# Optimization experiments

Measured on AMD Instinct MI355X. Metric: run time of the kernel, lower is better.

## Reference

```python
import jax, jax.numpy as jnp
import numpy as np

EMBED_DIM = 192
NUM_HEADS = 6
HEAD_DIM = EMBED_DIM // NUM_HEADS
WIN = (7, 7, 7)
N = WIN[0] * WIN[1] * WIN[2]  # 343
B = 512
NW = 64  # windows per volume (mask leading dim); B % NW == 0
SCALE = HEAD_DIM ** (-0.5)


def _relative_position_index():
    coords = np.stack(np.meshgrid(np.arange(WIN[0]), np.arange(WIN[1]), np.arange(WIN[2]), indexing='ij'))
    flat = coords.reshape(3, -1)
    rel = flat[:, :, None] - flat[:, None, :]            # (3, N, N)
    rel = np.transpose(rel, (1, 2, 0)).astype(np.int64)  # (N, N, 3)
    rel[:, :, 0] += WIN[0] - 1
    rel[:, :, 1] += WIN[1] - 1
    rel[:, :, 2] += WIN[2] - 1
    rel[:, :, 0] *= (2 * WIN[1] - 1) * (2 * WIN[2] - 1)
    rel[:, :, 1] *= 2 * WIN[2] - 1
    return rel.sum(-1)  # (N, N) ints in [0, (2Wh-1)(2Ww-1)(2Wd-1))


def setup_inputs() -> dict:
    key = jax.random.key(0)
    ks = jax.random.split(key, 7)
    table_size = (2 * WIN[0] - 1) * (2 * WIN[1] - 1) * (2 * WIN[2] - 1)  # 2197
    return {
        'x': jax.random.normal(ks[0], (B, N, EMBED_DIM), dtype=jnp.float32),
        'mask': jax.random.normal(ks[1], (NW, N, N), dtype=jnp.float32),
        'qkv_w': jax.random.normal(ks[2], (EMBED_DIM, 3 * EMBED_DIM), dtype=jnp.float32) * 0.02,
        'qkv_b': jnp.zeros((3 * EMBED_DIM,), dtype=jnp.float32),
        'proj_w': jax.random.normal(ks[3], (EMBED_DIM, EMBED_DIM), dtype=jnp.float32) * 0.02,
        'proj_b': jnp.zeros((EMBED_DIM,), dtype=jnp.float32),
        'bias_table': jax.random.normal(ks[4], (table_size, NUM_HEADS), dtype=jnp.float32) * 0.02,
        'rpi': jnp.asarray(_relative_position_index(), dtype=jnp.int32),  # (N, N)
    }


def reference(x, mask, qkv_w, qkv_b, proj_w, proj_b, bias_table, rpi):
    Bn, Nn, C = x.shape
    # QKV projection
    qkv = x @ qkv_w + qkv_b                                   # (B, N, 3C)
    qkv = qkv.reshape(Bn, Nn, 3, NUM_HEADS, HEAD_DIM)
    qkv = jnp.transpose(qkv, (2, 0, 3, 1, 4))                 # (3, B, H, N, hd)
    q, k, v = qkv[0], qkv[1], qkv[2]
    attn = jnp.einsum('bhnd,bhmd->bhnm', q * SCALE, k)        # (B, H, N, N)
    # gather relative position bias: (N*N, H) -> (1, H, N, N)
    rel_bias = bias_table[rpi.reshape(-1)].reshape(Nn, Nn, NUM_HEADS)
    attn = attn + jnp.transpose(rel_bias, (2, 0, 1))[None]
    # per-window mask addition
    nw = mask.shape[0]
    attn = attn.reshape(Bn // nw, nw, NUM_HEADS, Nn, Nn)
    attn = attn + mask[None, :, None, :, :]
    attn = attn.reshape(Bn, NUM_HEADS, Nn, Nn)
    attn = jax.nn.softmax(attn, axis=-1)
    out = jnp.einsum('bhnm,bhmd->bnhd', attn, v).reshape(Bn, Nn, C)
    return out @ proj_w + proj_b
```

## Files before the change

kernel.cpp:

```cpp
#include <hip/hip_runtime.h>
#include <stdint.h>

#define N_TOK 343
#define NPAD  352
#define EMB   192
#define HD    32
#define SCALE 0.17677669529663689f

typedef __attribute__((ext_vector_type(8))) short short8;
typedef __attribute__((ext_vector_type(4))) short short4v;
typedef __attribute__((ext_vector_type(4))) float floatx4;

__device__ __forceinline__ short f2bf(float f) {
  union { float f; unsigned u; } v; v.f = f;
  unsigned r = v.u + 0x7fffu + ((v.u >> 16) & 1u);
  return (short)(r >> 16);
}
__device__ __forceinline__ float bf2f(short s) {
  union { unsigned u; float f; } v;
  v.u = ((unsigned)(unsigned short)s) << 16;
  return v.f;
}
__device__ __forceinline__ unsigned pack2(float a, float b) {
  return (unsigned)(unsigned short)f2bf(a) | ((unsigned)(unsigned short)f2bf(b) << 16);
}

__global__ void prep_weights(const float* __restrict__ qkv_w,
                             const float* __restrict__ qkv_b,
                             const float* __restrict__ proj_w,
                             short* __restrict__ wpack,
                             float* __restrict__ bpack,
                             short* __restrict__ WpT)
{
  int i0 = blockIdx.x * blockDim.x + threadIdx.x;
  int stride = gridDim.x * blockDim.x;
  for (int idx = i0; idx < 110592; idx += stride) {
    int k = idx % 192;
    int t = idx / 192;
    int n = t % 32;
    int mat = (t / 32) % 3;
    int h = t / 96;
    float v = qkv_w[k * 576 + mat * 192 + h * 32 + n];
    if (mat == 0) v *= SCALE;
    wpack[idx] = f2bf(v);
  }
  for (int idx = i0; idx < 36864; idx += stride) {
    int k = idx % 192;
    int n = idx / 192;
    WpT[idx] = f2bf(proj_w[k * 192 + n]);
  }
  for (int idx = i0; idx < 576; idx += stride) {
    int d = idx % 32;
    int mat = (idx / 32) % 3;
    int h = idx / 96;
    float v = qkv_b[mat * 192 + h * 32 + d];
    if (mat == 0) v *= SCALE;
    bpack[idx] = v;
  }
}

__global__ void prep_bias(const float* __restrict__ bias_table,
                          const int* __restrict__ rpi,
                          short* __restrict__ biasH)
{
  int p = blockIdx.x * blockDim.x + threadIdx.x;
  int h = blockIdx.y;
  if (p < N_TOK * N_TOK) {
    int t = rpi[p];
    biasH[h * (N_TOK * N_TOK) + p] = f2bf(bias_table[t * 6 + h]);
  }
}

__global__ __launch_bounds__(256, 2) void fused_attn(
    const float* __restrict__ x,
    const float* __restrict__ mask,
    const short* __restrict__ wpack,
    const float* __restrict__ bpack,
    const short* __restrict__ biasH,
    short* __restrict__ AO)
{
  const int tid  = threadIdx.x;
  const int wave = tid >> 6;
  const int lane = tid & 63;
  const int l16  = lane & 15;
  const int quad = lane >> 4;

  int id   = blockIdx.x;
  int xcd  = id & 7;
  int j    = id >> 3;
  int w_id = xcd * 8 + (j / 48);
  int r    = j % 48;
  int h    = r % 6;
  int b    = (r / 6) * 64 + w_id;

  extern __shared__ short smem_s[];
  short* Kl = smem_s;
  short* Vt = smem_s + 14080;
  short* Wv = smem_s + 25600 + wave * 2048;
  short* Qs = Wv;
  short* Pb = Wv + 640;

  const float* bsrc = bpack + h * 96;
  const float bq0 = bsrc[l16],      bq1 = bsrc[16 + l16];
  const float bk0 = bsrc[32 + l16], bk1 = bsrc[48 + l16];
  const float bv0 = bsrc[64 + l16], bv1 = bsrc[80 + l16];

  const float* xb = x + (size_t)b * (N_TOK * EMB);
  const short* wh = wpack + h * 18432;
  unsigned qreg[6][4];

#pragma unroll 1
  for (int ch = 0; ch < 6; ++ch) {
    int r0 = ch * 64 + wave * 16;
    if (r0 >= NPAD) continue;
    int row = r0 + l16;
    bool rok = row < N_TOK;
    const float* xr = xb + (size_t)row * EMB;

    short8 af[6];
#pragma unroll
    for (int kk = 0; kk < 6; ++kk) {
      const float* xp = xr + kk * 32 + quad * 8;
      float4 a0 = rok ? *(const float4*)xp       : make_float4(0.f, 0.f, 0.f, 0.f);
      float4 a1 = rok ? *(const float4*)(xp + 4) : make_float4(0.f, 0.f, 0.f, 0.f);
      short8 t;
      t[0] = f2bf(a0.x); t[1] = f2bf(a0.y); t[2] = f2bf(a0.z); t[3] = f2bf(a0.w);
      t[4] = f2bf(a1.x); t[5] = f2bf(a1.y); t[6] = f2bf(a1.z); t[7] = f2bf(a1.w);
      af[kk] = t;
    }

    int mg = r0 + quad * 4;
#pragma unroll
    for (int mat = 0; mat < 3; ++mat) {
      const short* wb = wh + mat * 6144;
      floatx4 acc0 = {0.f, 0.f, 0.f, 0.f}, acc1 = {0.f, 0.f, 0.f, 0.f};
#pragma unroll
      for (int kk = 0; kk < 6; ++kk) {
        short8 b0 = *(const short8*)(wb + l16 * 192 + kk * 32 + quad * 8);
        short8 b1 = *(const short8*)(wb + (16 + l16) * 192 + kk * 32 + quad * 8);
        acc0 = __builtin_amdgcn_mfma_f32_16x16x32_bf16(af[kk], b0, acc0, 0, 0, 0);
        acc1 = __builtin_amdgcn_mfma_f32_16x16x32_bf16(af[kk], b1, acc1, 0, 0, 0);
      }
      if (mat == 0) {
#pragma unroll
        for (int reg = 0; reg < 4; ++reg)
          qreg[ch][reg] = pack2(acc0[reg] + bq0, acc1[reg] + bq1);
      } else if (mat == 1) {
#pragma unroll
        for (int reg = 0; reg < 4; ++reg) {
          int m = mg + reg;
          bool mv = m < N_TOK;
          Kl[m * 40 + l16]      = f2bf(mv ? acc0[reg] + bk0 : 0.f);
          Kl[m * 40 + 16 + l16] = f2bf(mv ? acc1[reg] + bk1 : 0.f);
        }
      } else {
        short4v sv0, sv1;
#pragma unroll
        for (int reg = 0; reg < 4; ++reg) {
          int m = mg + reg;
          bool mv = m < N_TOK;
          sv0[reg] = f2bf(mv ? acc0[reg] + bv0 : 0.f);
          sv1[reg] = f2bf(mv ? acc1[reg] + bv1 : 0.f);
        }
        *(short4v*)(Vt + l16 * 360 + mg)        = sv0;
        *(short4v*)(Vt + (16 + l16) * 360 + mg) = sv1;
      }
    }
  }
  __syncthreads();

  const float* mbase = mask + (size_t)(b & 63) * (N_TOK * N_TOK);
  const short* bbase = biasH + (size_t)h * (N_TOK * N_TOK);

#pragma unroll 1
  for (int c = wave; c < 22; c += 4) {
    const int m0 = c * 16;
    const int jx = c >> 2;

#pragma unroll
    for (int reg = 0; reg < 4; ++reg) {
      unsigned p = qreg[jx][reg];
      int rr = quad * 4 + reg;
      Qs[rr * 40 + l16]      = (short)(p & 0xffffu);
      Qs[rr * 40 + 16 + l16] = (short)(p >> 16);
    }
    short8 qf = *(const short8*)(Qs + l16 * 40 + quad * 8);

    const float* mr[4];
    const short* br[4];
#pragma unroll
    for (int reg = 0; reg < 4; ++reg) {
      int m = m0 + quad * 4 + reg;
      int mc = (m < N_TOK) ? m : (N_TOK - 1);
      mr[reg] = mbase + mc * N_TOK;
      br[reg] = bbase + mc * N_TOK;
    }

    float rsum4[4] = {0.f, 0.f, 0.f, 0.f};
    floatx4 o0 = {0.f, 0.f, 0.f, 0.f}, o1 = {0.f, 0.f, 0.f, 0.f};

    float nm0[4], nm1[4], nb0[4], nb1[4];
#pragma unroll
    for (int reg = 0; reg < 4; ++reg) {
      nm0[reg] = mr[reg][l16];
      nm1[reg] = mr[reg][16 + l16];
      nb0[reg] = bf2f(br[reg][l16]);
      nb1[reg] = bf2f(br[reg][16 + l16]);
    }

#pragma unroll 2
    for (int g = 0; g < 11; ++g) {
      float xm0[4], xm1[4], xb0[4], xb1[4];
#pragma unroll
      for (int reg = 0; reg < 4; ++reg) {
        xm0[reg] = nm0[reg]; xm1[reg] = nm1[reg];
        xb0[reg] = nb0[reg]; xb1[reg] = nb1[reg];
      }
      if (g < 10) {
        int c0 = (g + 1) * 32 + l16;
        int c1t = (g + 1) * 32 + 16 + l16;
        int c1 = (c1t < N_TOK) ? c1t : (N_TOK - 1);
#pragma unroll
        for (int reg = 0; reg < 4; ++reg) {
          nm0[reg] = mr[reg][c0];
          nm1[reg] = mr[reg][c1];
          nb0[reg] = bf2f(br[reg][c0]);
          nb1[reg] = bf2f(br[reg][c1]);
        }
      }

      const int k0 = g * 32;
      short8 kf0 = *(const short8*)(Kl + (k0 + l16) * 40 + quad * 8);
      short8 kf1 = *(const short8*)(Kl + (k0 + 16 + l16) * 40 + quad * 8);
      floatx4 zz = {0.f, 0.f, 0.f, 0.f};
      floatx4 s0 = __builtin_amdgcn_mfma_f32_16x16x32_bf16(qf, kf0, zz, 0, 0, 0);
      floatx4 s1 = __builtin_amdgcn_mfma_f32_16x16x32_bf16(qf, kf1, zz, 0, 0, 0);

      bool p1ok = (k0 + 16 + l16) < N_TOK;
      short* pb = Pb + (g & 1) * 640;
#pragma unroll
      for (int reg = 0; reg < 4; ++reg) {
        float e0 = exp2f((s0[reg] + xm0[reg] + xb0[reg]) * 1.44269504f);
        float e1 = p1ok ? exp2f((s1[reg] + xm1[reg] + xb1[reg]) * 1.44269504f) : 0.f;
        rsum4[reg] += e0 + e1;
        int rr = quad * 4 + reg;
        pb[rr * 40 + l16]      = f2bf(e0);
        pb[rr * 40 + 16 + l16] = f2bf(e1);
      }
      short8 pf  = *(const short8*)(pb + l16 * 40 + quad * 8);
      short8 vf0 = *(const short8*)(Vt + l16 * 360 + k0 + quad * 8);
      short8 vf1 = *(const short8*)(Vt + (16 + l16) * 360 + k0 + quad * 8);
      o0 = __builtin_amdgcn_mfma_f32_16x16x32_bf16(pf, vf0, o0, 0, 0, 0);
      o1 = __builtin_amdgcn_mfma_f32_16x16x32_bf16(pf, vf1, o1, 0, 0, 0);
    }

#pragma unroll
    for (int reg = 0; reg < 4; ++reg) {
      float s = rsum4[reg];
#pragma unroll
      for (int off = 1; off < 16; off <<= 1)
        s += __shfl_xor(s, off, 16);
      rsum4[reg] = 1.0f / s;
    }

#pragma unroll
    for (int reg = 0; reg < 4; ++reg) {
      int m = m0 + quad * 4 + reg;
      if (m < N_TOK) {
        short* dst = AO + ((size_t)b * N_TOK + m) * EMB + h * HD;
        dst[l16]      = f2bf(o0[reg] * rsum4[reg]);
        dst[16 + l16] = f2bf(o1[reg] * rsum4[reg]);
      }
    }
  }
}

__global__ __launch_bounds__(256) void proj_gemm(
    const short* __restrict__ AO,
    const short* __restrict__ WpT,
    const float* __restrict__ proj_b,
    float* __restrict__ out)
{
  __shared__ short As[64 * 200];
  const int tid  = threadIdx.x;
  const int wave = tid >> 6;
  const int lane = tid & 63;
  const int l16  = lane & 15;
  const int quad = lane >> 4;
  const int mb = blockIdx.x;

  const short* Ab = AO + (size_t)mb * (64 * EMB);
  for (int i = tid * 8; i < 64 * EMB; i += 2048) {
    uint4 va = *(const uint4*)(Ab + i);
    int rr = i / EMB, cc = i - rr * EMB;
    *(uint4*)(As + rr * 200 + cc) = va;
  }
  __syncthreads();

  short8 af[6];
#pragma unroll
  for (int kk = 0; kk < 6; ++kk)
    af[kk] = *(const short8*)(As + (wave * 16 + l16) * 200 + kk * 32 + quad * 8);

#pragma unroll 1
  for (int nt = 0; nt < 12; ++nt) {
    floatx4 acc = {0.f, 0.f, 0.f, 0.f};
#pragma unroll
    for (int kk = 0; kk < 6; ++kk) {
      short8 bf = *(const short8*)(WpT + (nt * 16 + l16) * EMB + kk * 32 + quad * 8);
      acc = __builtin_amdgcn_mfma_f32_16x16x32_bf16(af[kk], bf, acc, 0, 0, 0);
    }
    int colg = nt * 16 + l16;
    float pb = proj_b[colg];
    int mrow = mb * 64 + wave * 16 + quad * 4;
#pragma unroll
    for (int reg = 0; reg < 4; ++reg) {
      out[(size_t)(mrow + reg) * EMB + colg] = acc[reg] + pb;
    }
  }
}

extern "C" void kernel_launch(void* const* d_in, const int* in_sizes, int n_in,
                              void* d_out, int out_size, void* d_ws, size_t ws_size,
                              hipStream_t stream) {
  (void)in_sizes; (void)n_in; (void)out_size; (void)ws_size;
  const float* x        = (const float*)d_in[0];
  const float* mask     = (const float*)d_in[1];
  const float* qkv_w    = (const float*)d_in[2];
  const float* qkv_b    = (const float*)d_in[3];
  const float* proj_w   = (const float*)d_in[4];
  const float* proj_b   = (const float*)d_in[5];
  const float* bias_tab = (const float*)d_in[6];
  const int*   rpi      = (const int*)d_in[7];

  char* ws = (char*)d_ws;
  short* wpack = (short*)(ws);
  float* bpack = (float*)(ws + 221184);
  short* WpT   = (short*)(ws + 223488);
  short* biasH = (short*)(ws + 297216);
  short* AO    = (short*)(ws + 1709056);

  hipLaunchKernelGGL(prep_weights, dim3(128), dim3(256), 0, stream,
                     qkv_w, qkv_b, proj_w, wpack, bpack, WpT);
  hipLaunchKernelGGL(prep_bias, dim3(460, 6), dim3(256), 0, stream,
                     bias_tab, rpi, biasH);

  const int lds_bytes = 67584;
  (void)hipFuncSetAttribute((const void*)fused_attn,
                            hipFuncAttributeMaxDynamicSharedMemorySize, lds_bytes);
  hipLaunchKernelGGL(fused_attn, dim3(3072), dim3(256), lds_bytes, stream,
                     x, mask, wpack, bpack, biasH, AO);

  hipLaunchKernelGGL(proj_gemm, dim3(2744), dim3(256), 0, stream,
                     AO, WpT, proj_b, (float*)d_out);
}
```

Measured before the change: 903.2 us.

## Use 8 waves per attention block and drop LDS staging in projection GEMM

The fused attention kernel now runs 512 threads (8 waves) per block. Each wave handles fewer 16-row chunks, and the Q and P scratch space per wave is shared and shrunk so LDS stays near its previous size. The projection GEMM stops staging A tiles through shared memory: each wave loads two 16-row A tiles directly from global memory and reuses each B fragment across two MFMAs, so half as many blocks are launched. The aim is more latency hiding in attention and less LDS and sync overhead in the projection. The risks are tighter register limits under launch_bounds(512,4) and possible hazards from aliasing the Q and P scratch buffers.

After: 1.314 ms. +45.5%, slower.

```diff
diff --git a/kernel.cpp b/kernel.cpp
--- a/kernel.cpp
+++ b/kernel.cpp
@@ -71,7 +71,7 @@
   }
 }
 
-__global__ __launch_bounds__(256, 2) void fused_attn(
+__global__ __launch_bounds__(512, 4) void fused_attn(
     const float* __restrict__ x,
     const float* __restrict__ mask,
     const short* __restrict__ wpack,
@@ -96,9 +96,9 @@
   extern __shared__ short smem_s[];
   short* Kl = smem_s;
   short* Vt = smem_s + 14080;
-  short* Wv = smem_s + 25600 + wave * 2048;
+  short* Wv = smem_s + 25600 + wave * 1280;
   short* Qs = Wv;
-  short* Pb = Wv + 640;
+  short* Pb = Wv;
 
   const float* bsrc = bpack + h * 96;
   const float bq0 = bsrc[l16],      bq1 = bsrc[16 + l16];
@@ -107,11 +107,11 @@
 
   const float* xb = x + (size_t)b * (N_TOK * EMB);
   const short* wh = wpack + h * 18432;
-  unsigned qreg[6][4];
+  unsigned qreg[3][4];
 
 #pragma unroll 1
-  for (int ch = 0; ch < 6; ++ch) {
-    int r0 = ch * 64 + wave * 16;
+  for (int ch = 0; ch < 3; ++ch) {
+    int r0 = (ch * 8 + wave) * 16;
     if (r0 >= NPAD) continue;
     int row = r0 + l16;
     bool rok = row < N_TOK;
@@ -173,9 +173,9 @@
   const short* bbase = biasH + (size_t)h * (N_TOK * N_TOK);
 
 #pragma unroll 1
-  for (int c = wave; c < 22; c += 4) {
+  for (int c = wave; c < 22; c += 8) {
     const int m0 = c * 16;
-    const int jx = c >> 2;
+    const int jx = c >> 3;
 
 #pragma unroll
     for (int reg = 0; reg < 4; ++reg) {
@@ -281,41 +281,40 @@
     const float* __restrict__ proj_b,
     float* __restrict__ out)
 {
-  __shared__ short As[64 * 200];
   const int tid  = threadIdx.x;
   const int wave = tid >> 6;
   const int lane = tid & 63;
   const int l16  = lane & 15;
   const int quad = lane >> 4;
-  const int mb = blockIdx.x;
-
-  const short* Ab = AO + (size_t)mb * (64 * EMB);
-  for (int i = tid * 8; i < 64 * EMB; i += 2048) {
-    uint4 va = *(const uint4*)(Ab + i);
-    int rr = i / EMB, cc = i - rr * EMB;
-    *(uint4*)(As + rr * 200 + cc) = va;
-  }
-  __syncthreads();
-
-  short8 af[6];
-#pragma unroll
-  for (int kk = 0; kk < 6; ++kk)
-    af[kk] = *(const short8*)(As + (wave * 16 + l16) * 200 + kk * 32 + quad * 8);
+  const int mt2 = blockIdx.x * 4 + wave;
+  const int ta = mt2 * 2, tb = ta + 1;
+
+  const short* Aa = AO + (size_t)ta * 16 * EMB + l16 * EMB + quad * 8;
+  const short* Ab = AO + (size_t)tb * 16 * EMB + l16 * EMB + quad * 8;
+  short8 af0[6], af1[6];
+#pragma unroll
+  for (int kk = 0; kk < 6; ++kk) {
+    af0[kk] = *(const short8*)(Aa + kk * 32);
+    af1[kk] = *(const short8*)(Ab + kk * 32);
+  }
 
 #pragma unroll 1
   for (int nt = 0; nt < 12; ++nt) {
-    floatx4 acc = {0.f, 0.f, 0.f, 0.f};
+    floatx4 acc0 = {0.f, 0.f, 0.f, 0.f}, acc1 = {0.f, 0.f, 0.f, 0.f};
 #pragma unroll
     for (int kk = 0; kk < 6; ++kk) {
       short8 bf = *(const short8*)(WpT + (nt * 16 + l16) * EMB + kk * 32 + quad * 8);
-      acc = __builtin_amdgcn_mfma_f32_16x16x32_bf16(af[kk], bf, acc, 0, 0, 0);
+      acc0 = __builtin_amdgcn_mfma_f32_16x16x32_bf16(af0[kk], bf, acc0, 0, 0, 0);
+      acc1 = __builtin_amdgcn_mfma_f32_16x16x32_bf16(af1[kk], bf, acc1, 0, 0, 0);
     }
     int colg = nt * 16 + l16;
     float pb = proj_b[colg];
-    int mrow = mb * 64 + wave * 16 + quad * 4;
-#pragma unroll
-    for (int reg = 0; reg < 4; ++reg) {
-      out[(size_t)(mrow + reg) * EMB + colg] = acc[reg] + pb;
+    int ra = ta * 16 + quad * 4;
+    int rb = tb * 16 + quad * 4;
+#pragma unroll
+    for (int reg = 0; reg < 4; ++reg) {
+      out[(size_t)(ra + reg) * EMB + colg] = acc0[reg] + pb;
+      out[(size_t)(rb + reg) * EMB + colg] = acc1[reg] + pb;
     }
   }
 }
@@ -345,12 +344,12 @@
   hipLaunchKernelGGL(prep_bias, dim3(460, 6), dim3(256), 0, stream,
                      bias_tab, rpi, biasH);
 
-  const int lds_bytes = 67584;
+  const int lds_bytes = 71680;
   (void)hipFuncSetAttribute((const void*)fused_attn,
                             hipFuncAttributeMaxDynamicSharedMemorySize, lds_bytes);
-  hipLaunchKernelGGL(fused_attn, dim3(3072), dim3(256), lds_bytes, stream,
+  hipLaunchKernelGGL(fused_attn, dim3(3072), dim3(512), lds_bytes, stream,
                      x, mask, wpack, bpack, biasH, AO);
 
-  hipLaunchKernelGGL(proj_gemm, dim3(2744), dim3(256), 0, stream,
+  hipLaunchKernelGGL(proj_gemm, dim3(1372), dim3(256), 0, stream,
                      AO, WpT, proj_b, (float*)d_out);
 }
```
